# Kernel optimization log

Hardware: AMD Instinct MI355X
Metric: run time of the kernel (lower is better)

The kernel has to match this reference:

```python
import jax, jax.numpy as jnp
import numpy as np

K = 512
D = 256


def setup_inputs() -> dict:
    key = jax.random.key(0)
    k1, k2 = jax.random.split(key)
    x = jax.random.normal(k1, (64, D, 32, 32), dtype=jnp.float32)
    # nn.Embedding(K, D) init: uniform(-1/K, 1/K)
    emb = jax.random.uniform(k2, (K, D), dtype=jnp.float32, minval=-1.0 / K, maxval=1.0 / K)
    return {"x": x, "emb": emb}


def reference(x, emb):
    # encoder is identity: z_e_x = x, shape [B, D, H, W]
    B, Dd, H, W = x.shape
    z_e = jnp.transpose(x, (0, 2, 3, 1))           # [B, H, W, D]
    z_flat = z_e.reshape(-1, Dd)                    # [N, D]
    # squared euclidean distances to codebook: ||z||^2 + ||e||^2 - 2 z.e
    dist = (jnp.sum(z_flat * z_flat, axis=1, keepdims=True)
            + jnp.sum(emb * emb, axis=1)[None, :]
            - 2.0 * z_flat @ emb.T)                 # [N, K]
    idx = jnp.argmin(dist, axis=1)                  # [N]
    codes = emb[idx]                                # [N, D] gather
    codes = codes.reshape(B, H, W, Dd)
    # straight-through quantized output (value == codes)
    z_q_st = z_e + jax.lax.stop_gradient(codes - z_e)
    z_q_st = jnp.transpose(z_q_st, (0, 3, 1, 2))    # [B, D, H, W]
    # z_q_x_bar: gathered from live codebook (grads flow to emb)
    z_q_bar = jnp.transpose(codes, (0, 3, 1, 2))    # [B, D, H, W]
    # decoder is identity: x_tilde = z_q_st
    return (z_q_st, x, z_q_bar)
```

## Files before the change

### kernel.cpp

```cpp
#include <hip/hip_runtime.h>


#define B_  64
#define D_  256
#define HW_ 1024
#define K_  512

typedef __attribute__((ext_vector_type(8))) short short8;
typedef __attribute__((ext_vector_type(4))) float f32x4;

__device__ unsigned short g_ebf[K_ * D_];
__device__ float g_e2[K_];

__device__ __forceinline__ unsigned short f2bf(float f) {
    unsigned u = __float_as_uint(f);
    u += 0x7fffu + ((u >> 16) & 1u);
    return (unsigned short)(u >> 16);
}

__global__ void prep(const float* __restrict__ emb) {
    const int t   = threadIdx.x;
    const int row = blockIdx.x * 8 + (t >> 5);
    const int c0  = (t & 31) * 8;
    const float* rp = emb + row * D_ + c0;
    float4 a = *(const float4*)rp;
    float4 b = *(const float4*)(rp + 4);
    short8 v;
    v[0] = (short)f2bf(a.x); v[1] = (short)f2bf(a.y);
    v[2] = (short)f2bf(a.z); v[3] = (short)f2bf(a.w);
    v[4] = (short)f2bf(b.x); v[5] = (short)f2bf(b.y);
    v[6] = (short)f2bf(b.z); v[7] = (short)f2bf(b.w);
    *(short8*)(g_ebf + row * D_ + c0) = v;
    float ps = a.x*a.x + a.y*a.y + a.z*a.z + a.w*a.w
             + b.x*b.x + b.y*b.y + b.z*b.z + b.w*b.w;
    ps += __shfl_xor(ps, 1);  ps += __shfl_xor(ps, 2);
    ps += __shfl_xor(ps, 4);  ps += __shfl_xor(ps, 8);
    ps += __shfl_xor(ps, 16);
    if ((t & 31) == 0) g_e2[row] = ps;
}

__global__ __launch_bounds__(256, 2)
void vq_main(const float* __restrict__ x, const float* __restrict__ emb,
             float* __restrict__ out0, float* __restrict__ out1,
             float* __restrict__ out2) {
    __shared__ float zc[4][32][36];
    __shared__ int   idxs[128];

    const int t   = threadIdx.x;
    const int w   = t >> 6;
    const int l   = t & 63;
    const int blk = blockIdx.x;
    const int b   = blk >> 3;
    const int hw0 = (blk & 7) << 7;
    const float* xb = x    + ((size_t)b * D_) * HW_ + hw0;
    float*       o1 = out1 + ((size_t)b * D_) * HW_ + hw0;
    const int hwb = w * 32;

    short8 zb[2][8];
    for (int g = 0; g < 8; ++g) {
#pragma unroll
        for (int it = 0; it < 4; ++it) {
            const int d2 = 8 * it + (l >> 3);
            const int dr = 32 * g + d2;
            const int cc = (l & 7) * 4;
            float4 v = *(const float4*)&xb[(size_t)dr * HW_ + hwb + cc];
            *(float4*)&o1[(size_t)dr * HW_ + hwb + cc] = v;
            *(float4*)&zc[w][d2][cc] = v;
        }
        __syncthreads();
#pragma unroll
        for (int t2 = 0; t2 < 2; ++t2) {
            const int p = 16 * t2 + (l & 15);
            short8 f;
#pragma unroll
            for (int j = 0; j < 8; ++j)
                f[j] = (short)f2bf(zc[w][(l >> 4) * 8 + j][p]);
            zb[t2][g] = f;
        }
        __syncthreads();
    }

    float minv0 = 3.0e38f, minv1 = 3.0e38f;
    int   mini0 = 0,       mini1 = 0;
    short8 ea[8], eb[8];
    f32x4  e2a, e2b;

#define LOADE(buf, e2r, ct) do {                                              \
        const unsigned short* _p = g_ebf + ((ct) * 16 + (l & 15)) * D_        \
                                   + (l >> 4) * 8;                            \
        _Pragma("unroll")                                                     \
        for (int s = 0; s < 8; ++s) buf[s] = *(const short8*)(_p + s * 32);   \
        e2r = *(const f32x4*)(g_e2 + (ct) * 16 + (l >> 4) * 4);               \
    } while (0)

#define PROC(buf, e2v, ct) do {                                               \
        f32x4 a0 = {0.f, 0.f, 0.f, 0.f}, a1 = {0.f, 0.f, 0.f, 0.f};          \
        _Pragma("unroll")                                                     \
        for (int s = 0; s < 8; ++s) {                                         \
            a0 = __builtin_amdgcn_mfma_f32_16x16x32_bf16(buf[s], zb[0][s], a0, 0, 0, 0); \
            a1 = __builtin_amdgcn_mfma_f32_16x16x32_bf16(buf[s], zb[1][s], a1, 0, 0, 0); \
        }                                                                     \
        _Pragma("unroll")                                                     \
        for (int r = 0; r < 4; ++r) {                                         \
            const int code = (ct) * 16 + (l >> 4) * 4 + r;                    \
            const float s0 = e2v[r] - 2.0f * a0[r];                           \
            const float s1 = e2v[r] - 2.0f * a1[r];                           \
            if (s0 < minv0) { minv0 = s0; mini0 = code; }                     \
            if (s1 < minv1) { minv1 = s1; mini1 = code; }                     \
        }                                                                     \
    } while (0)

    LOADE(ea, e2a, 0);
    for (int c = 0; c < 32; c += 2) {
        LOADE(eb, e2b, c + 1);
        PROC(ea, e2a, c);
        const int cn = (c + 2 < 32) ? (c + 2) : 0;
        LOADE(ea, e2a, cn);
        PROC(eb, e2b, c + 1);
    }

    {
        float ov; int oi;
        ov = __shfl_xor(minv0, 16); oi = __shfl_xor(mini0, 16);
        if (ov < minv0 || (ov == minv0 && oi < mini0)) { minv0 = ov; mini0 = oi; }
        ov = __shfl_xor(minv0, 32); oi = __shfl_xor(mini0, 32);
        if (ov < minv0 || (ov == minv0 && oi < mini0)) { minv0 = ov; mini0 = oi; }
        ov = __shfl_xor(minv1, 16); oi = __shfl_xor(mini1, 16);
        if (ov < minv1 || (ov == minv1 && oi < mini1)) { minv1 = ov; mini1 = oi; }
        ov = __shfl_xor(minv1, 32); oi = __shfl_xor(mini1, 32);
        if (ov < minv1 || (ov == minv1 && oi < mini1)) { minv1 = ov; mini1 = oi; }
    }
    if ((l >> 4) == 0) {
        idxs[w * 32 + (l & 15)]      = mini0;
        idxs[w * 32 + 16 + (l & 15)] = mini1;
    }
    __syncthreads();

    {
        const int n  = t & 127;
        const int dg = t >> 7;
        const float* erow = emb + (size_t)idxs[n] * D_;
        float* p0 = out0 + ((size_t)b * D_) * HW_ + hw0 + n;
        float* p2 = out2 + ((size_t)b * D_) * HW_ + hw0 + n;
#pragma unroll 4
        for (int i = 0; i < 32; ++i) {
            const int d = dg * 4 + i * 8;
            float4 v = *(const float4*)&erow[d];
            p0[(size_t)(d + 0) * HW_] = v.x; p0[(size_t)(d + 1) * HW_] = v.y;
            p0[(size_t)(d + 2) * HW_] = v.z; p0[(size_t)(d + 3) * HW_] = v.w;
            p2[(size_t)(d + 0) * HW_] = v.x; p2[(size_t)(d + 1) * HW_] = v.y;
            p2[(size_t)(d + 2) * HW_] = v.z; p2[(size_t)(d + 3) * HW_] = v.w;
        }
    }
}

extern "C" void kernel_launch(void* const* d_in, const int* in_sizes, int n_in,
                              void* d_out, int out_size, void* d_ws, size_t ws_size,
                              hipStream_t stream) {
    const float* x   = (const float*)d_in[0];
    const float* emb = (const float*)d_in[1];
    float* out0 = (float*)d_out;
    float* out1 = out0 + (size_t)16777216;
    float* out2 = out0 + (size_t)33554432;

    prep<<<64, 256, 0, stream>>>(emb);
    vq_main<<<512, 256, 0, stream>>>(x, emb, out0, out1, out2);
}
```

Before: 302.9 us.

## Split codebook search across two waves per 32-pixel block with async LDS loads

Each block now handles 32 pixels with 2 waves instead of 128 pixels with 4 waves, and the two waves each scan half of the codebook. Their partial argmins are merged through shared memory. Input tiles are staged with global_load_lds direct-to-LDS loads, and the out1 copy is written back from LDS. The aim is more blocks for occupancy and load balance, plus less register traffic on the input path. The cost is that each pixel's x data is converted to bf16 by both waves, and there is an extra sync and reduction step.

```diff
diff --git a/kernel.cpp b/kernel.cpp
--- a/kernel.cpp
+++ b/kernel.cpp
@@ -39,43 +39,62 @@
     if ((t & 31) == 0) g_e2[row] = ps;
 }
 
-__global__ __launch_bounds__(256, 2)
+__global__ __launch_bounds__(128, 4)
 void vq_main(const float* __restrict__ x, const float* __restrict__ emb,
              float* __restrict__ out0, float* __restrict__ out1,
              float* __restrict__ out2) {
-    __shared__ float zc[4][32][36];
-    __shared__ int   idxs[128];
+    __shared__ float zc[4][32][32];
+    __shared__ float mval[2][32];
+    __shared__ int   midx[2][32];
+    __shared__ int   fidx[32];
 
     const int t   = threadIdx.x;
     const int w   = t >> 6;
     const int l   = t & 63;
     const int blk = blockIdx.x;
-    const int b   = blk >> 3;
-    const int hw0 = (blk & 7) << 7;
+    const int b   = blk >> 5;
+    const int hw0 = (blk & 31) << 5;
     const float* xb = x    + ((size_t)b * D_) * HW_ + hw0;
     float*       o1 = out1 + ((size_t)b * D_) * HW_ + hw0;
-    const int hwb = w * 32;
 
     short8 zb[2][8];
-    for (int g = 0; g < 8; ++g) {
+    for (int r = 0; r < 2; ++r) {
 #pragma unroll
-        for (int it = 0; it < 4; ++it) {
-            const int d2 = 8 * it + (l >> 3);
-            const int dr = 32 * g + d2;
-            const int cc = (l & 7) * 4;
-            float4 v = *(const float4*)&xb[(size_t)dr * HW_ + hwb + cc];
-            *(float4*)&o1[(size_t)dr * HW_ + hwb + cc] = v;
-            *(float4*)&zc[w][d2][cc] = v;
+        for (int gg = 0; gg < 2; ++gg) {
+            const int g = 4 * r + 2 * w + gg;
+#pragma unroll
+            for (int it = 0; it < 4; ++it) {
+                const float* gp = xb + (size_t)(32 * g + 8 * it + (l >> 3)) * HW_ + (l & 7) * 4;
+                float* lp = &zc[g & 3][8 * it][0];
+                __builtin_amdgcn_global_load_lds(
+                    (const __attribute__((address_space(1))) unsigned int*)gp,
+                    (__attribute__((address_space(3))) unsigned int*)lp,
+                    16, 0, 0);
+            }
         }
         __syncthreads();
 #pragma unroll
-        for (int t2 = 0; t2 < 2; ++t2) {
-            const int p = 16 * t2 + (l & 15);
-            short8 f;
+        for (int g4 = 0; g4 < 4; ++g4) {
+            const int g = 4 * r + g4;
 #pragma unroll
-            for (int j = 0; j < 8; ++j)
-                f[j] = (short)f2bf(zc[w][(l >> 4) * 8 + j][p]);
-            zb[t2][g] = f;
+            for (int t2 = 0; t2 < 2; ++t2) {
+                const int p = 16 * t2 + (l & 15);
+                short8 f;
+#pragma unroll
+                for (int j = 0; j < 8; ++j)
+                    f[j] = (short)f2bf(zc[g4][(l >> 4) * 8 + j][p]);
+                zb[t2][g] = f;
+            }
+        }
+#pragma unroll
+        for (int gg = 0; gg < 2; ++gg) {
+            const int g = 4 * r + 2 * w + gg;
+#pragma unroll
+            for (int it = 0; it < 4; ++it) {
+                const int dr = 32 * g + 8 * it + (l >> 3);
+                float4 v = *(const float4*)&zc[g & 3][8 * it + (l >> 3)][(l & 7) * 4];
+                *(float4*)&o1[(size_t)dr * HW_ + (l & 7) * 4] = v;
+            }
         }
         __syncthreads();
     }
@@ -84,6 +103,7 @@
     int   mini0 = 0,       mini1 = 0;
     short8 ea[8], eb[8];
     f32x4  e2a, e2b;
+    const int ctbase = w * 16;
 
 #define LOADE(buf, e2r, ct) do {                                              \
         const unsigned short* _p = g_ebf + ((ct) * 16 + (l & 15)) * D_        \
@@ -110,13 +130,13 @@
         }                                                                     \
     } while (0)
 
-    LOADE(ea, e2a, 0);
-    for (int c = 0; c < 32; c += 2) {
-        LOADE(eb, e2b, c + 1);
-        PROC(ea, e2a, c);
-        const int cn = (c + 2 < 32) ? (c + 2) : 0;
+    LOADE(ea, e2a, ctbase);
+    for (int c = 0; c < 16; c += 2) {
+        LOADE(eb, e2b, ctbase + c + 1);
+        PROC(ea, e2a, ctbase + c);
+        const int cn = (c + 2 < 16) ? (ctbase + c + 2) : ctbase;
         LOADE(ea, e2a, cn);
-        PROC(eb, e2b, c + 1);
+        PROC(eb, e2b, ctbase + c + 1);
     }
 
     {
@@ -131,20 +151,25 @@
         if (ov < minv1 || (ov == minv1 && oi < mini1)) { minv1 = ov; mini1 = oi; }
     }
     if ((l >> 4) == 0) {
-        idxs[w * 32 + (l & 15)]      = mini0;
-        idxs[w * 32 + 16 + (l & 15)] = mini1;
+        mval[w][l & 15]      = minv0; midx[w][l & 15]      = mini0;
+        mval[w][16 + (l & 15)] = minv1; midx[w][16 + (l & 15)] = mini1;
+    }
+    __syncthreads();
+    if (t < 32) {
+        const float v0 = mval[0][t], v1 = mval[1][t];
+        fidx[t] = (v1 < v0) ? midx[1][t] : midx[0][t];
     }
     __syncthreads();
 
     {
-        const int n  = t & 127;
-        const int dg = t >> 7;
-        const float* erow = emb + (size_t)idxs[n] * D_;
+        const int n  = t & 31;
+        const int dg = t >> 5;
+        const float* erow = emb + (size_t)fidx[n] * D_;
         float* p0 = out0 + ((size_t)b * D_) * HW_ + hw0 + n;
         float* p2 = out2 + ((size_t)b * D_) * HW_ + hw0 + n;
 #pragma unroll 4
-        for (int i = 0; i < 32; ++i) {
-            const int d = dg * 4 + i * 8;
+        for (int i = 0; i < 16; ++i) {
+            const int d = dg * 4 + i * 16;
             float4 v = *(const float4*)&erow[d];
             p0[(size_t)(d + 0) * HW_] = v.x; p0[(size_t)(d + 1) * HW_] = v.y;
             p0[(size_t)(d + 2) * HW_] = v.z; p0[(size_t)(d + 3) * HW_] = v.w;
@@ -164,5 +189,5 @@
     float* out2 = out0 + (size_t)33554432;
 
     prep<<<64, 256, 0, stream>>>(emb);
-    vq_main<<<512, 256, 0, stream>>>(x, emb, out0, out1, out2);
+    vq_main<<<2048, 128, 0, stream>>>(x, emb, out0, out1, out2);
 }
```

Result: slower. 314.1 us (+3.7%).
